# Optimization experiments

Measured on AMD Instinct MI355X. Metric: run time of the kernel, lower is better.

Reference implementation:

```python
import jax, jax.numpy as jnp
import numpy as np
import math

B, D, NH, NS, NT = 16, 256, 512, 8, 32
NV = NS * NT          # 256 prediction variables
L, H, A = 4, 8, 64    # attention layers, heads, head dim
HA = H * A            # 512
M = 512               # mlp_dim
R = 128               # resolution
EPS = 1e-5


def setup_inputs() -> dict:
    key = jax.random.key(0)
    ks = jax.random.split(key, 32)
    s = 0.02
    inp = {
        'hist_encoded': jax.random.normal(ks[0], (B, NH, D), jnp.float32),
        'hist_true_u': jax.random.uniform(ks[1], (B, NH), jnp.float32),
        'pred_encoded': jax.random.normal(ks[2], (B, NV, D), jnp.float32),
        'pred_true_u': jax.random.uniform(ks[3], (B, NV), jnp.float32),
        # dimension shifting layer
        'ds_w': jax.random.normal(ks[4], (D, HA), jnp.float32) * s,
        'ds_b': jnp.zeros((HA,), jnp.float32),
        # per-layer, per-head key/value creators: Linear(D+1 -> A)
        'key_w': jax.random.normal(ks[5], (L, H, D + 1, A), jnp.float32) * s,
        'key_b': jnp.zeros((L, H, A), jnp.float32),
        'val_w': jax.random.normal(ks[6], (L, H, D + 1, A), jnp.float32) * s,
        'val_b': jnp.zeros((L, H, A), jnp.float32),
        # layer norms
        'ln1_g': jnp.ones((L, HA), jnp.float32),
        'ln1_b': jnp.zeros((L, HA), jnp.float32),
        'ln2_g': jnp.ones((L, HA), jnp.float32),
        'ln2_b': jnp.zeros((L, HA), jnp.float32),
        # feed-forward (mlp_layers=2): HA->M, M->M, M->HA
        'ff_w1': jax.random.normal(ks[7], (L, HA, M), jnp.float32) * s,
        'ff_b1': jnp.zeros((L, M), jnp.float32),
        'ff_w2': jax.random.normal(ks[8], (L, M, M), jnp.float32) * s,
        'ff_b2': jnp.zeros((L, M), jnp.float32),
        'ff_w3': jax.random.normal(ks[9], (L, M, HA), jnp.float32) * s,
        'ff_b3': jnp.zeros((L, HA), jnp.float32),
        # dist extractor
        'de_w': jax.random.normal(ks[10], (HA, R), jnp.float32) * s,
        'de_b': jnp.zeros((R,), jnp.float32),
        'num_series': NS,
        'num_timesteps': NT,
    }
    return inp


def _ln(x, g, b):
    m = x.mean(-1, keepdims=True)
    v = ((x - m) ** 2).mean(-1, keepdims=True)
    return g * (x - m) / jnp.sqrt(v + EPS) + b


def _forward(hist_encoded, hist_true_u, pred_encoded, pred_true_u,
             ds_w, ds_b, key_w, key_b, val_w, val_b,
             ln1_g, ln1_b, ln2_g, ln2_b,
             ff_w1, ff_b1, ff_w2, ff_b2, ff_w3, ff_b3,
             de_w, de_b):
    Bm, NVm, Dm = pred_encoded.shape
    NHm = hist_encoded.shape[1]
    Lm, Hm, _, Am = key_w.shape
    W = NHm + NVm
    # identity permutation in the source loss() -> no-op
    att = pred_encoded @ ds_w + ds_b  # [B, NV, HA]
    # key/value inputs: [hist||u ; pred||u] -> [B, W, D+1]
    ki = jnp.concatenate([
        jnp.concatenate([hist_encoded, hist_true_u[:, :, None]], axis=2),
        jnp.concatenate([pred_encoded, pred_true_u[:, :, None]], axis=2)], axis=1)
    keys = jnp.einsum('bwd,lhda->lbhwa', ki, key_w) + key_b[:, None, :, None, :]
    vals = jnp.einsum('bwd,lhda->lbhwa', ki, val_w) + val_b[:, None, :, None, :]
    # flipped-triangular mask: position w is masked iff w >= NH + v
    mask = jnp.arange(W)[None, :] >= (NHm + jnp.arange(NVm)[:, None])  # [NV, W]
    scale = Am ** (-0.5)
    for l in range(Lm):
        avh = att.reshape(Bm, NVm, Hm, Am)
        prod = jnp.einsum('bvhi,bhwi->bhvw', avh, keys[l])  # [B,H,NV,W]
        prod = jnp.where(mask, -jnp.inf, prod) * scale
        w = jax.nn.softmax(prod, axis=-1)
        a = jnp.einsum('bhvw,bhwj->bvhj', w, vals[l]).reshape(Bm, NVm, Hm * Am)
        att = _ln(att + a, ln1_g[l], ln1_b[l])
        ff = jnp.maximum(att @ ff_w1[l] + ff_b1[l], 0.0)
        ff = jnp.maximum(ff @ ff_w2[l] + ff_b2[l], 0.0)
        ff = ff @ ff_w3[l] + ff_b3[l]
        att = _ln(att + ff, ln2_g[l], ln2_b[l])
    res = de_w.shape[-1]
    target = jnp.clip(jnp.floor(pred_true_u[:, 1:] * res).astype(jnp.int32), 0, res - 1)
    logits = (att @ de_w + de_b)[:, 1:, :]
    lp = math.log(res) + jax.nn.log_softmax(logits, axis=2)
    lp = jnp.take_along_axis(lp, target[:, :, None], axis=2)[:, :, 0]
    return -lp.sum(axis=1)  # [B]


def reference(hist_encoded, hist_true_u, pred_encoded, pred_true_u,
              ds_w, ds_b, key_w, key_b, val_w, val_b,
              ln1_g, ln1_b, ln2_g, ln2_b,
              ff_w1, ff_b1, ff_w2, ff_b2, ff_w3, ff_b3,
              de_w, de_b, num_series, num_timesteps):
    assert pred_encoded.shape[1] == num_series * num_timesteps
    return _forward(hist_encoded, hist_true_u, pred_encoded, pred_true_u,
                    ds_w, ds_b, key_w, key_b, val_w, val_b,
                    ln1_g, ln1_b, ln2_g, ln2_b,
                    ff_w1, ff_b1, ff_w2, ff_b2, ff_w3, ff_b3,
                    de_w, de_b)
```

## Files before the change

kernel.cpp:

```cpp
#include <hip/hip_runtime.h>

constexpr int kB = 16, kD = 256, kNH = 512, kNV = 256, kW = 768;
constexpr int kL = 4, kH = 8, kA = 64, kHA = 512, kM = 512, kR = 128;
constexpr int kKP = 288;

typedef __bf16 bf16x8 __attribute__((ext_vector_type(8)));
typedef __bf16 bf16x4 __attribute__((ext_vector_type(4)));
typedef float f32x4 __attribute__((ext_vector_type(4)));

__device__ inline void load_lds16(const __bf16* g, __bf16* l) {
  __builtin_amdgcn_global_load_lds(
      (const __attribute__((address_space(1))) void*)g,
      (__attribute__((address_space(3))) void*)l, 16, 0, 0);
}

constexpr int kP1 = kB * kW * kKP;
constexpr int kP2 = 4096 * kKP;
constexpr int kP3 = 12 * 512 * 512;
constexpr int kP4 = 200704;
constexpr int kPT = kP1 + kP2 + kP3 + kP4;

__global__ void prep_kernel(const float* __restrict__ hist,
                            const float* __restrict__ hist_u,
                            const float* __restrict__ pred,
                            const float* __restrict__ pred_u,
                            const float* __restrict__ kw,
                            const float* __restrict__ vw,
                            const float* __restrict__ w1,
                            const float* __restrict__ w2,
                            const float* __restrict__ w3,
                            const float* __restrict__ ds_w,
                            const float* __restrict__ de_w,
                            const float* __restrict__ key_b,
                            const float* __restrict__ val_b,
                            __bf16* __restrict__ ki,
                            __bf16* __restrict__ kvwt,
                            __bf16* __restrict__ ffwt,
                            __bf16* __restrict__ ds_wt,
                            __bf16* __restrict__ de_wt,
                            float* __restrict__ kvb) {
  int i = blockIdx.x * 256 + threadIdx.x;
  if (i < kP1) {
    int d = i % kKP;
    int bw = i / kKP;
    int w = bw % kW;
    int b = bw / kW;
    float v = 0.f;
    if (d < 257) {
      if (w < kNH)
        v = (d < kD) ? hist[((size_t)b * kNH + w) * kD + d] : hist_u[b * kNH + w];
      else {
        int p = w - kNH;
        v = (d < kD) ? pred[((size_t)b * kNV + p) * kD + d] : pred_u[b * kNV + p];
      }
    }
    ki[i] = (__bf16)v;
  } else if (i < kP1 + kP2) {
    int j = i - kP1;
    int d = j % kKP;
    int c = j / kKP;
    float v = 0.f;
    if (d < 257) {
      bool isv = c >= 2048;
      int cc = isv ? c - 2048 : c;
      int l = cc >> 9, rest = cc & 511;
      int h = rest >> 6, a = rest & 63;
      size_t src = (((size_t)l * kH + h) * 257 + d) * kA + a;
      v = isv ? vw[src] : kw[src];
    }
    kvwt[j] = (__bf16)v;
  } else if (i < kP1 + kP2 + kP3) {
    int j = i - kP1 - kP2;
    int k = j & 511;
    int n = (j >> 9) & 511;
    int mat = j >> 18;
    int l = mat / 3, which = mat % 3;
    const float* src = which == 0 ? w1 : which == 1 ? w2 : w3;
    ffwt[j] = (__bf16)src[((size_t)l * 512 + k) * 512 + n];
  } else if (i < kPT) {
    int j = i - kP1 - kP2 - kP3;
    if (j < 131072) {
      int n = j >> 8, k = j & 255;
      ds_wt[j] = (__bf16)ds_w[k * 512 + n];
    } else if (j < 196608) {
      int jj = j - 131072;
      int n = jj >> 9, k = jj & 511;
      de_wt[jj] = (__bf16)de_w[k * 128 + n];
    } else {
      int c = j - 196608;
      bool isv = c >= 2048;
      int cc = isv ? c - 2048 : c;
      int l = cc >> 9, rest = cc & 511;
      kvb[c] = isv ? val_b[l * 512 + rest] : key_b[l * 512 + rest];
    }
  }
}

template <int BN, int OMODE, bool RELU, bool KIMAP, bool BIASROW>
__global__ __launch_bounds__(256) void gemm_mfma_kernel(
    const __bf16* __restrict__ A, const __bf16* __restrict__ Bt,
    const float* __restrict__ bias, void* __restrict__ Cout,
    __bf16* __restrict__ Cout2, int M, int N, int K, int lda, int ldc) {
  constexpr int JN = BN / 32;
  constexpr int BROWS = BN / 4;
  __shared__ __bf16 As[128 * 32];
  __shared__ __bf16 Bs[BN * 32];
  const int t = threadIdx.x;
  const int wid = t >> 6;
  const int lane = t & 63;
  const int bm = blockIdx.y * 128;
  const int bn = blockIdx.x * BN;
  const int wm = (wid >> 1) * 64;
  const int wn = (wid & 1) * (BN / 2);
  const int sr = lane >> 2, sc = lane & 3;
  const int skey = (sr >> 1) & 3;
  const int abase = KIMAP ? ((bm >> 8) * 768 + 512 + (bm & 255)) : bm;
  const __bf16* Ag = A + (size_t)(abase + wid * 32 + sr) * lda + (sc ^ skey) * 8;
  const __bf16* Bg = Bt + (size_t)(bn + wid * BROWS + sr) * K + (sc ^ skey) * 8;
  __bf16* AsW = As + (wid * 32) * 32;
  __bf16* BsW = Bs + (wid * BROWS) * 32;

  f32x4 acc[4][JN] = {};
  const int q = lane >> 4, mr = lane & 15;
  const int rkey = (mr >> 1) & 3;
  for (int k0 = 0; k0 < K; k0 += 32) {
    if (k0) __syncthreads();
    load_lds16(Ag + k0, AsW);
    load_lds16(Ag + (size_t)16 * lda + k0, AsW + 16 * 32);
    load_lds16(Bg + k0, BsW);
    if (BN == 128) load_lds16(Bg + (size_t)16 * K + k0, BsW + 16 * 32);
    __syncthreads();
    bf16x8 af[4], bfr[JN];
#pragma unroll
    for (int i = 0; i < 4; ++i)
      af[i] = *(const bf16x8*)(As + (wm + i * 16 + mr) * 32 + (q ^ rkey) * 8);
#pragma unroll
    for (int j = 0; j < JN; ++j)
      bfr[j] = *(const bf16x8*)(Bs + (wn + j * 16 + mr) * 32 + (q ^ rkey) * 8);
#pragma unroll
    for (int i = 0; i < 4; ++i)
#pragma unroll
      for (int j = 0; j < JN; ++j)
        acc[i][j] = __builtin_amdgcn_mfma_f32_16x16x32_bf16(af[i], bfr[j],
                                                            acc[i][j], 0, 0, 0);
  }
#pragma unroll
  for (int j = 0; j < JN; ++j) {
    int col = bn + wn + j * 16 + mr;
    float bscol = BIASROW ? 0.f : bias[col];
#pragma unroll
    for (int i = 0; i < 4; ++i) {
      int row0 = bm + wm + i * 16 + q * 4;
#pragma unroll
      for (int r = 0; r < 4; ++r) {
        float v = acc[i][j][r] + (BIASROW ? bias[row0 + r] : bscol);
        if (RELU) v = fmaxf(v, 0.f);
        size_t idx = (size_t)(row0 + r) * ldc + col;
        if (OMODE == 0) {
          ((float*)Cout)[idx] = v;
        } else if (OMODE == 1) {
          ((__bf16*)Cout)[idx] = (__bf16)v;
        } else {
          ((float*)Cout)[idx] = v;
          Cout2[idx] = (__bf16)v;
        }
      }
    }
  }
}

__global__ __launch_bounds__(256) void attn_mfma_kernel(
    const __bf16* __restrict__ attbf, const __bf16* __restrict__ kvs_k,
    const __bf16* __restrict__ vT, __bf16* __restrict__ outbf, int l) {
  const int b = blockIdx.z, h = blockIdx.y, qt = blockIdx.x;
  __shared__ __bf16 Ks[64 * 72];
  __shared__ __bf16 Vt[64 * 72];
  __shared__ __bf16 Ps[64 * 72];
  const int t = threadIdx.x;
  const int w = t >> 6, lane = t & 63;
  const int quad = lane >> 4, mr = lane & 15;
  bf16x8 aq[2];
  {
    const __bf16* qp = attbf + ((size_t)(b * kNV + qt * 64 + w * 16 + mr) * kHA +
                                h * kA + quad * 8);
    aq[0] = *(const bf16x8*)qp;
    aq[1] = *(const bf16x8*)(qp + 32);
  }
  f32x4 o[4] = {};
  float m_ = -1e30f, l_ = 0.f;
  const int cmax = kNH + qt * 64;
  const int pr = t >> 2, pc = t & 3;
  const __bf16* kbase = kvs_k + ((size_t)(b * kW + pr) * 2048 + l * 512 + h * kA);
  const __bf16* vbase = vT + (size_t)(l * 512 + h * kA + pr) * 12288 + b * kW;
  bf16x8 kc0, kc1, vc0, vc1;
  kc0 = *(const bf16x8*)(kbase + pc * 8);
  kc1 = *(const bf16x8*)(kbase + pc * 8 + 32);
  vc0 = *(const bf16x8*)(vbase + pc * 16);
  vc1 = *(const bf16x8*)(vbase + pc * 16 + 8);
  for (int c0 = 0; c0 <= cmax; c0 += 64) {
    __syncthreads();
    *(bf16x8*)&Ks[pr * 72 + pc * 8] = kc0;
    *(bf16x8*)&Ks[pr * 72 + pc * 8 + 32] = kc1;
    *(bf16x8*)&Vt[pr * 72 + pc * 16] = vc0;
    *(bf16x8*)&Vt[pr * 72 + pc * 16 + 8] = vc1;
    __syncthreads();
    if (c0 + 64 <= cmax) {
      const __bf16* kp = kbase + (size_t)(c0 + 64) * 2048;
      const __bf16* vp = vbase + c0 + 64;
      kc0 = *(const bf16x8*)(kp + pc * 8);
      kc1 = *(const bf16x8*)(kp + pc * 8 + 32);
      vc0 = *(const bf16x8*)(vp + pc * 16);
      vc1 = *(const bf16x8*)(vp + pc * 16 + 8);
    }
    f32x4 s[4];
#pragma unroll
    for (int j = 0; j < 4; ++j) {
      bf16x8 ak0 = *(const bf16x8*)&Ks[(j * 16 + mr) * 72 + quad * 8];
      bf16x8 ak1 = *(const bf16x8*)&Ks[(j * 16 + mr) * 72 + quad * 8 + 32];
      f32x4 z = {};
      z = __builtin_amdgcn_mfma_f32_16x16x32_bf16(ak0, aq[0], z, 0, 0, 0);
      z = __builtin_amdgcn_mfma_f32_16x16x32_bf16(ak1, aq[1], z, 0, 0, 0);
      s[j] = z;
    }
    const int lim = cmax - c0;
    float sv[16], mx = -1e30f;
#pragma unroll
    for (int j = 0; j < 4; ++j)
#pragma unroll
      for (int r = 0; r < 4; ++r) {
        int p = j * 16 + quad * 4 + r;
        float x = (p < lim + mr) ? s[j][r] * 0.125f : -1e30f;
        sv[j * 4 + r] = x;
        mx = fmaxf(mx, x);
      }
    mx = fmaxf(mx, __shfl_xor(mx, 16));
    mx = fmaxf(mx, __shfl_xor(mx, 32));
    float mnew = fmaxf(m_, mx);
    float corr = __expf(m_ - mnew);
    float rs = 0.f;
#pragma unroll
    for (int i = 0; i < 16; ++i) {
      sv[i] = __expf(sv[i] - mnew);
      rs += sv[i];
    }
    rs += __shfl_xor(rs, 16);
    rs += __shfl_xor(rs, 32);
    l_ = l_ * corr + rs;
    m_ = mnew;
#pragma unroll
    for (int j = 0; j < 4; ++j) {
      bf16x4 pk = {(__bf16)sv[j * 4 + 0], (__bf16)sv[j * 4 + 1],
                   (__bf16)sv[j * 4 + 2], (__bf16)sv[j * 4 + 3]};
      *(bf16x4*)&Ps[(w * 16 + mr) * 72 + j * 16 + quad * 4] = pk;
    }
#pragma unroll
    for (int r = 0; r < 4; ++r) {
      float cr = __shfl(corr, quad * 4 + r);
#pragma unroll
      for (int j = 0; j < 4; ++j) o[j][r] *= cr;
    }
    bf16x8 ap0 = *(const bf16x8*)&Ps[(w * 16 + mr) * 72 + quad * 8];
    bf16x8 ap1 = *(const bf16x8*)&Ps[(w * 16 + mr) * 72 + quad * 8 + 32];
#pragma unroll
    for (int j = 0; j < 4; ++j) {
      bf16x8 b0 = *(const bf16x8*)&Vt[(j * 16 + mr) * 72 + quad * 8];
      bf16x8 b1 = *(const bf16x8*)&Vt[(j * 16 + mr) * 72 + quad * 8 + 32];
      o[j] = __builtin_amdgcn_mfma_f32_16x16x32_bf16(ap0, b0, o[j], 0, 0, 0);
      o[j] = __builtin_amdgcn_mfma_f32_16x16x32_bf16(ap1, b1, o[j], 0, 0, 0);
    }
  }
  float invl = 1.f / l_;
#pragma unroll
  for (int r = 0; r < 4; ++r) {
    float ir = __shfl(invl, quad * 4 + r);
    int row = b * kNV + qt * 64 + w * 16 + quad * 4 + r;
#pragma unroll
    for (int j = 0; j < 4; ++j)
      outbf[(size_t)row * kHA + h * kA + j * 16 + mr] = (__bf16)(o[j][r] * ir);
  }
}

__global__ __launch_bounds__(128) void add_ln_kernel(
    float* __restrict__ att, const __bf16* __restrict__ addbf,
    const float* __restrict__ g, const float* __restrict__ be,
    __bf16* __restrict__ attbf) {
  const int row = blockIdx.x;
  const int t = threadIdx.x;
  float4* ar = (float4*)(att + (size_t)row * kHA);
  bf16x4 dv = *(const bf16x4*)(addbf + (size_t)row * kHA + t * 4);
  float4 x = ar[t];
  x.x += (float)dv[0]; x.y += (float)dv[1];
  x.z += (float)dv[2]; x.w += (float)dv[3];
  float s = x.x + x.y + x.z + x.w;
  float sq = x.x * x.x + x.y * x.y + x.z * x.z + x.w * x.w;
  for (int o = 32; o; o >>= 1) {
    s += __shfl_xor(s, o);
    sq += __shfl_xor(sq, o);
  }
  __shared__ float red[4];
  if ((t & 63) == 0) { red[(t >> 6) * 2] = s; red[(t >> 6) * 2 + 1] = sq; }
  __syncthreads();
  float S = red[0] + red[2], Q = red[1] + red[3];
  float mean = S * (1.f / kHA);
  float inv = rsqrtf(Q * (1.f / kHA) - mean * mean + 1e-5f);
  float4 gv = ((const float4*)g)[t];
  float4 bv = ((const float4*)be)[t];
  float4 y;
  y.x = gv.x * (x.x - mean) * inv + bv.x;
  y.y = gv.y * (x.y - mean) * inv + bv.y;
  y.z = gv.z * (x.z - mean) * inv + bv.z;
  y.w = gv.w * (x.w - mean) * inv + bv.w;
  ar[t] = y;
  bf16x4 yb = {(__bf16)y.x, (__bf16)y.y, (__bf16)y.z, (__bf16)y.w};
  *(bf16x4*)(attbf + (size_t)row * kHA + t * 4) = yb;
}

__global__ __launch_bounds__(256) void de_loss_kernel(
    const __bf16* __restrict__ attbf, const __bf16* __restrict__ de_wt,
    const float* __restrict__ de_b, const float* __restrict__ pred_u,
    float* __restrict__ parts) {
  const int blk = blockIdx.x;
  const int t = threadIdx.x;
  const int w = t >> 6, lane = t & 63, quad = lane >> 4, mr = lane & 15;
  const int row0 = blk * 64 + w * 16;
  f32x4 acc[8] = {};
  const __bf16* Ap = attbf + (size_t)(row0 + mr) * kHA + quad * 8;
#pragma unroll 4
  for (int k0 = 0; k0 < 512; k0 += 32) {
    bf16x8 a = *(const bf16x8*)(Ap + k0);
#pragma unroll
    for (int j = 0; j < 8; ++j) {
      bf16x8 bb =
          *(const bf16x8*)(de_wt + (size_t)(j * 16 + mr) * 512 + k0 + quad * 8);
      acc[j] = __builtin_amdgcn_mfma_f32_16x16x32_bf16(a, bb, acc[j], 0, 0, 0);
    }
  }
  float dbv[8];
#pragma unroll
  for (int j = 0; j < 8; ++j) dbv[j] = de_b[j * 16 + mr];
  float lpacc = 0.f;
#pragma unroll
  for (int r = 0; r < 4; ++r) {
    int row = row0 + quad * 4 + r;
    int v = row & 255, bidx = row >> 8;
    float lg[8], mx = -1e30f;
#pragma unroll
    for (int j = 0; j < 8; ++j) {
      lg[j] = acc[j][r] + dbv[j];
      mx = fmaxf(mx, lg[j]);
    }
    mx = fmaxf(mx, __shfl_xor(mx, 1));
    mx = fmaxf(mx, __shfl_xor(mx, 2));
    mx = fmaxf(mx, __shfl_xor(mx, 4));
    mx = fmaxf(mx, __shfl_xor(mx, 8));
    float se = 0.f;
#pragma unroll
    for (int j = 0; j < 8; ++j) se += __expf(lg[j] - mx);
    se += __shfl_xor(se, 1);
    se += __shfl_xor(se, 2);
    se += __shfl_xor(se, 4);
    se += __shfl_xor(se, 8);
    float lse = mx + __logf(se);
    float u = pred_u[bidx * 256 + v];
    int tgt = (int)floorf(u * 128.f);
    tgt = max(0, min(127, tgt));
    float cand = (mr == (tgt & 15)) ? lg[tgt >> 4] : 0.f;
    cand += __shfl_xor(cand, 1);
    cand += __shfl_xor(cand, 2);
    cand += __shfl_xor(cand, 4);
    cand += __shfl_xor(cand, 8);
    float lp = (v >= 1) ? (4.8520302639196171f + cand - lse) : 0.f;
    lpacc += lp;
  }
  lpacc += __shfl_xor(lpacc, 16);
  lpacc += __shfl_xor(lpacc, 32);
  __shared__ float red[4];
  if (lane == 0) red[w] = lpacc;
  __syncthreads();
  if (t == 0) parts[blk] = red[0] + red[1] + red[2] + red[3];
}

__global__ void loss_final_kernel(const float* __restrict__ parts,
                                  float* __restrict__ out) {
  int b = threadIdx.x;
  if (b < kB)
    out[b] = -(parts[b * 4] + parts[b * 4 + 1] + parts[b * 4 + 2] +
               parts[b * 4 + 3]);
}

extern "C" void kernel_launch(void* const* d_in, const int* in_sizes, int n_in,
                              void* d_out, int out_size, void* d_ws, size_t ws_size,
                              hipStream_t stream) {
  const float* hist   = (const float*)d_in[0];
  const float* hist_u = (const float*)d_in[1];
  const float* pred   = (const float*)d_in[2];
  const float* pred_u = (const float*)d_in[3];
  const float* ds_w   = (const float*)d_in[4];
  const float* ds_b   = (const float*)d_in[5];
  const float* key_w  = (const float*)d_in[6];
  const float* key_b  = (const float*)d_in[7];
  const float* val_w  = (const float*)d_in[8];
  const float* val_b  = (const float*)d_in[9];
  const float* ln1_g  = (const float*)d_in[10];
  const float* ln1_b  = (const float*)d_in[11];
  const float* ln2_g  = (const float*)d_in[12];
  const float* ln2_b  = (const float*)d_in[13];
  const float* ff_w1  = (const float*)d_in[14];
  const float* ff_b1  = (const float*)d_in[15];
  const float* ff_w2  = (const float*)d_in[16];
  const float* ff_b2  = (const float*)d_in[17];
  const float* ff_w3  = (const float*)d_in[18];
  const float* ff_b3  = (const float*)d_in[19];
  const float* de_w   = (const float*)d_in[20];
  const float* de_b   = (const float*)d_in[21];
  float* out = (float*)d_out;

  char* ws = (char*)d_ws;
  size_t off = 0;
  auto alloc = [&](size_t bytes) { char* p = ws + off; off += bytes; return p; };
  __bf16* ki_bf  = (__bf16*)alloc((size_t)kB * kW * kKP * 2);
  __bf16* kv_wt  = (__bf16*)alloc((size_t)4096 * kKP * 2);
  __bf16* ffw_t  = (__bf16*)alloc((size_t)12 * 512 * 512 * 2);
  __bf16* ds_wt  = (__bf16*)alloc((size_t)512 * 256 * 2);
  __bf16* de_wt  = (__bf16*)alloc((size_t)128 * 512 * 2);
  float*  kvb    = (float*)alloc((size_t)4096 * 4);
  __bf16* kvs_k  = (__bf16*)alloc((size_t)kB * kW * 2048 * 2);
  __bf16* vT     = (__bf16*)alloc((size_t)2048 * 12288 * 2);
  float*  att    = (float*)alloc((size_t)kB * kNV * kHA * 4);
  __bf16* att_bf = (__bf16*)alloc((size_t)kB * kNV * kHA * 2);
  __bf16* tmp_bf = (__bf16*)alloc((size_t)kB * kNV * kHA * 2);
  __bf16* ff1_bf = (__bf16*)alloc((size_t)kB * kNV * kM * 2);
  __bf16* ff2_bf = (__bf16*)alloc((size_t)kB * kNV * kM * 2);
  float*  parts  = (float*)alloc(64 * 4);

  prep_kernel<<<(kPT + 255) / 256, 256, 0, stream>>>(
      hist, hist_u, pred, pred_u, key_w, val_w, ff_w1, ff_w2, ff_w3, ds_w, de_w,
      key_b, val_b, ki_bf, kv_wt, ffw_t, ds_wt, de_wt, kvb);

  gemm_mfma_kernel<64, 2, false, true, false>
      <<<dim3(kHA / 64, kB * kNV / 128), 256, 0, stream>>>(
          ki_bf, ds_wt, ds_b, att, att_bf, kB * kNV, kHA, kD, kKP, kHA);

  gemm_mfma_kernel<128, 1, false, false, false>
      <<<dim3(2048 / 128, kB * kW / 128), 256, 0, stream>>>(
          ki_bf, kv_wt, kvb, kvs_k, nullptr, kB * kW, 2048, kKP, kKP, 2048);
  gemm_mfma_kernel<128, 1, false, false, true>
      <<<dim3(kB * kW / 128, 2048 / 128), 256, 0, stream>>>(
          kv_wt + (size_t)2048 * kKP, ki_bf, kvb + 2048, vT, nullptr, 2048,
          kB * kW, kKP, kKP, kB * kW);

  for (int l = 0; l < kL; ++l) {
    attn_mfma_kernel<<<dim3(kNV / 64, kH, kB), 256, 0, stream>>>(
        att_bf, kvs_k, vT, tmp_bf, l);
    add_ln_kernel<<<kB * kNV, 128, 0, stream>>>(att, tmp_bf, ln1_g + l * kHA,
                                                ln1_b + l * kHA, att_bf);
    gemm_mfma_kernel<64, 1, true, false, false>
        <<<dim3(kM / 64, kB * kNV / 128), 256, 0, stream>>>(
            att_bf, ffw_t + (size_t)(l * 3) * 262144, ff_b1 + l * kM, ff1_bf,
            nullptr, kB * kNV, kM, kHA, kHA, kM);
    gemm_mfma_kernel<64, 1, true, false, false>
        <<<dim3(kM / 64, kB * kNV / 128), 256, 0, stream>>>(
            ff1_bf, ffw_t + (size_t)(l * 3 + 1) * 262144, ff_b2 + l * kM, ff2_bf,
            nullptr, kB * kNV, kM, kM, kM, kM);
    gemm_mfma_kernel<64, 1, false, false, false>
        <<<dim3(kHA / 64, kB * kNV / 128), 256, 0, stream>>>(
            ff2_bf, ffw_t + (size_t)(l * 3 + 2) * 262144, ff_b3 + l * kHA, tmp_bf,
            nullptr, kB * kNV, kHA, kM, kM, kHA);
    add_ln_kernel<<<kB * kNV, 128, 0, stream>>>(att, tmp_bf, ln2_g + l * kHA,
                                                ln2_b + l * kHA, att_bf);
  }
  de_loss_kernel<<<64, 256, 0, stream>>>(att_bf, de_wt, de_b, pred_u, parts);
  loss_final_kernel<<<1, 64, 0, stream>>>(parts, out);
}
```

Before: 492.3 us.

## Fuse layer norms into neighboring kernels via atomic row statistics

Removes the standalone add+layernorm kernels. Residual adds now happen in the attention and FF3 epilogues, which accumulate per-row sum and sum-of-squares with atomics. Normalization is applied lazily when the next consumer (attention query load, FF1 A-operand, loss kernel) reads the fp32 state, and the three initial projection GEMMs are merged into one launch. This cuts launches and bf16 round-trip traffic, at the cost of recomputing normalization in operand loads, FF1 reading fp32 A directly from global without LDS staging, and variance computed as E[x^2]-m^2.

```diff
diff --git a/kernel.cpp b/kernel.cpp
--- a/kernel.cpp
+++ b/kernel.cpp
@@ -3,6 +3,7 @@
 constexpr int kB = 16, kD = 256, kNH = 512, kNV = 256, kW = 768;
 constexpr int kL = 4, kH = 8, kA = 64, kHA = 512, kM = 512, kR = 128;
 constexpr int kKP = 288;
+constexpr int kRows = kB * kNV;
 
 typedef __bf16 bf16x8 __attribute__((ext_vector_type(8)));
 typedef __bf16 bf16x4 __attribute__((ext_vector_type(4)));
@@ -18,7 +19,8 @@
 constexpr int kP2 = 4096 * kKP;
 constexpr int kP3 = 12 * 512 * 512;
 constexpr int kP4 = 200704;
-constexpr int kPT = kP1 + kP2 + kP3 + kP4;
+constexpr int kP5 = 65536;
+constexpr int kPT = kP1 + kP2 + kP3 + kP4 + kP5;
 
 __global__ void prep_kernel(const float* __restrict__ hist,
                             const float* __restrict__ hist_u,
@@ -38,7 +40,8 @@
                             __bf16* __restrict__ ffwt,
                             __bf16* __restrict__ ds_wt,
                             __bf16* __restrict__ de_wt,
-                            float* __restrict__ kvb) {
+                            float* __restrict__ kvb,
+                            float* __restrict__ stats) {
   int i = blockIdx.x * 256 + threadIdx.x;
   if (i < kP1) {
     int d = i % kKP;
@@ -77,7 +80,7 @@
     int l = mat / 3, which = mat % 3;
     const float* src = which == 0 ? w1 : which == 1 ? w2 : w3;
     ffwt[j] = (__bf16)src[((size_t)l * 512 + k) * 512 + n];
-  } else if (i < kPT) {
+  } else if (i < kP1 + kP2 + kP3 + kP4) {
     int j = i - kP1 - kP2 - kP3;
     if (j < 131072) {
       int n = j >> 8, k = j & 255;
@@ -93,23 +96,24 @@
       int l = cc >> 9, rest = cc & 511;
       kvb[c] = isv ? val_b[l * 512 + rest] : key_b[l * 512 + rest];
     }
+  } else if (i < kPT) {
+    stats[i - kP1 - kP2 - kP3 - kP4] = 0.f;
   }
 }
 
 template <int BN, int OMODE, bool RELU, bool KIMAP, bool BIASROW>
-__global__ __launch_bounds__(256) void gemm_mfma_kernel(
-    const __bf16* __restrict__ A, const __bf16* __restrict__ Bt,
-    const float* __restrict__ bias, void* __restrict__ Cout,
-    __bf16* __restrict__ Cout2, int M, int N, int K, int lda, int ldc) {
+__device__ __forceinline__ void gemm_core(
+    int bxv, int byv, const __bf16* __restrict__ A,
+    const __bf16* __restrict__ Bt, const float* __restrict__ bias,
+    void* __restrict__ Cout, int K, int lda, int ldc,
+    __bf16* As, __bf16* Bs) {
   constexpr int JN = BN / 32;
   constexpr int BROWS = BN / 4;
-  __shared__ __bf16 As[128 * 32];
-  __shared__ __bf16 Bs[BN * 32];
   const int t = threadIdx.x;
   const int wid = t >> 6;
   const int lane = t & 63;
-  const int bm = blockIdx.y * 128;
-  const int bn = blockIdx.x * BN;
+  const int bm = byv * 128;
+  const int bn = bxv * BN;
   const int wm = (wid >> 1) * 64;
   const int wn = (wid & 1) * (BN / 2);
   const int sr = lane >> 2, sc = lane & 3;
@@ -156,22 +160,45 @@
         float v = acc[i][j][r] + (BIASROW ? bias[row0 + r] : bscol);
         if (RELU) v = fmaxf(v, 0.f);
         size_t idx = (size_t)(row0 + r) * ldc + col;
-        if (OMODE == 0) {
+        if (OMODE == 0)
           ((float*)Cout)[idx] = v;
-        } else if (OMODE == 1) {
+        else
           ((__bf16*)Cout)[idx] = (__bf16)v;
-        } else {
-          ((float*)Cout)[idx] = v;
-          Cout2[idx] = (__bf16)v;
-        }
       }
     }
   }
 }
 
-__global__ __launch_bounds__(256) void attn_mfma_kernel(
-    const __bf16* __restrict__ attbf, const __bf16* __restrict__ kvs_k,
-    const __bf16* __restrict__ vT, __bf16* __restrict__ outbf, int l) {
+__global__ __launch_bounds__(256) void gemm3_kernel(
+    const __bf16* __restrict__ ki, const __bf16* __restrict__ ds_wt,
+    const float* __restrict__ ds_b, float* __restrict__ S,
+    const __bf16* __restrict__ kv_wt, const float* __restrict__ kvb,
+    __bf16* __restrict__ kvs_k, __bf16* __restrict__ vT) {
+  __shared__ __bf16 smem[8192];
+  __bf16* As = smem;
+  __bf16* Bs = smem + 4096;
+  int bid = blockIdx.x;
+  if (bid < 256) {
+    gemm_core<64, 0, false, true, false>(bid & 7, bid >> 3, ki, ds_wt, ds_b, S,
+                                         256, kKP, 512, As, Bs);
+  } else if (bid < 1792) {
+    int b2 = bid - 256;
+    gemm_core<128, 1, false, false, false>(b2 & 15, b2 >> 4, ki, kv_wt, kvb,
+                                           kvs_k, kKP, kKP, 2048, As, Bs);
+  } else {
+    int b3 = bid - 1792;
+    gemm_core<128, 1, false, false, true>(b3 % 96, b3 / 96,
+                                          kv_wt + (size_t)2048 * kKP, ki,
+                                          kvb + 2048, vT, kKP, kKP, 12288, As,
+                                          Bs);
+  }
+}
+
+__global__ __launch_bounds__(256) void attn_kernel(
+    float* __restrict__ S, const __bf16* __restrict__ kvs_k,
+    const __bf16* __restrict__ vT, const float* __restrict__ statsPrev,
+    float* __restrict__ statsA, const float* __restrict__ g2,
+    const float* __restrict__ b2, int l) {
   const int b = blockIdx.z, h = blockIdx.y, qt = blockIdx.x;
   __shared__ __bf16 Ks[64 * 72];
   __shared__ __bf16 Vt[64 * 72];
@@ -181,10 +208,30 @@
   const int quad = lane >> 4, mr = lane & 15;
   bf16x8 aq[2];
   {
-    const __bf16* qp = attbf + ((size_t)(b * kNV + qt * 64 + w * 16 + mr) * kHA +
-                                h * kA + quad * 8);
-    aq[0] = *(const bf16x8*)qp;
-    aq[1] = *(const bf16x8*)(qp + 32);
+    int row = b * kNV + qt * 64 + w * 16 + mr;
+    const float* sp = S + (size_t)row * kHA + h * kA + quad * 8;
+    float4 x0 = *(const float4*)sp;
+    float4 x1 = *(const float4*)(sp + 4);
+    float4 x2 = *(const float4*)(sp + 32);
+    float4 x3 = *(const float4*)(sp + 36);
+    float xs[16] = {x0.x, x0.y, x0.z, x0.w, x1.x, x1.y, x1.z, x1.w,
+                    x2.x, x2.y, x2.z, x2.w, x3.x, x3.y, x3.z, x3.w};
+    if (l > 0) {
+      float s0 = statsPrev[2 * row], s1 = statsPrev[2 * row + 1];
+      float m = s0 * (1.f / kHA);
+      float inv = rsqrtf(s1 * (1.f / kHA) - m * m + 1e-5f);
+      int cbase = h * kA + quad * 8;
+#pragma unroll
+      for (int e = 0; e < 8; ++e) {
+        xs[e] = (xs[e] - m) * inv * g2[cbase + e] + b2[cbase + e];
+        xs[8 + e] = (xs[8 + e] - m) * inv * g2[cbase + 32 + e] + b2[cbase + 32 + e];
+      }
+    }
+#pragma unroll
+    for (int e = 0; e < 8; ++e) {
+      aq[0][e] = (__bf16)xs[e];
+      aq[1][e] = (__bf16)xs[8 + e];
+    }
   }
   f32x4 o[4] = {};
   float m_ = -1e30f, l_ = 0.f;
@@ -274,60 +321,248 @@
   for (int r = 0; r < 4; ++r) {
     float ir = __shfl(invl, quad * 4 + r);
     int row = b * kNV + qt * 64 + w * 16 + quad * 4 + r;
-#pragma unroll
-    for (int j = 0; j < 4; ++j)
-      outbf[(size_t)row * kHA + h * kA + j * 16 + mr] = (__bf16)(o[j][r] * ir);
-  }
-}
-
-__global__ __launch_bounds__(128) void add_ln_kernel(
-    float* __restrict__ att, const __bf16* __restrict__ addbf,
+    float m = 0.f, inv = 0.f;
+    if (l > 0) {
+      float s0 = statsPrev[2 * row], s1 = statsPrev[2 * row + 1];
+      m = s0 * (1.f / kHA);
+      inv = rsqrtf(s1 * (1.f / kHA) - m * m + 1e-5f);
+    }
+    float ps = 0.f, pq = 0.f;
+#pragma unroll
+    for (int j = 0; j < 4; ++j) {
+      int col = h * kA + j * 16 + mr;
+      size_t idx = (size_t)row * kHA + col;
+      float sval = S[idx];
+      float base = (l > 0) ? ((sval - m) * inv * g2[col] + b2[col]) : sval;
+      float v = base + o[j][r] * ir;
+      S[idx] = v;
+      ps += v;
+      pq += v * v;
+    }
+    ps += __shfl_xor(ps, 1); pq += __shfl_xor(pq, 1);
+    ps += __shfl_xor(ps, 2); pq += __shfl_xor(pq, 2);
+    ps += __shfl_xor(ps, 4); pq += __shfl_xor(pq, 4);
+    ps += __shfl_xor(ps, 8); pq += __shfl_xor(pq, 8);
+    if (mr == 0) {
+      atomicAdd(&statsA[2 * row], ps);
+      atomicAdd(&statsA[2 * row + 1], pq);
+    }
+  }
+}
+
+__global__ __launch_bounds__(256) void ff1_ln_gemm_kernel(
+    const float* __restrict__ S, const float* __restrict__ stats,
     const float* __restrict__ g, const float* __restrict__ be,
-    __bf16* __restrict__ attbf) {
-  const int row = blockIdx.x;
+    const __bf16* __restrict__ Bt, const float* __restrict__ bias,
+    __bf16* __restrict__ Cout) {
+  __shared__ __bf16 Bs[64 * 32];
+  __shared__ float gb[1024];
   const int t = threadIdx.x;
-  float4* ar = (float4*)(att + (size_t)row * kHA);
-  bf16x4 dv = *(const bf16x4*)(addbf + (size_t)row * kHA + t * 4);
-  float4 x = ar[t];
-  x.x += (float)dv[0]; x.y += (float)dv[1];
-  x.z += (float)dv[2]; x.w += (float)dv[3];
-  float s = x.x + x.y + x.z + x.w;
-  float sq = x.x * x.x + x.y * x.y + x.z * x.z + x.w * x.w;
-  for (int o = 32; o; o >>= 1) {
-    s += __shfl_xor(s, o);
-    sq += __shfl_xor(sq, o);
-  }
-  __shared__ float red[4];
-  if ((t & 63) == 0) { red[(t >> 6) * 2] = s; red[(t >> 6) * 2 + 1] = sq; }
+  for (int i = t; i < 512; i += 256) {
+    gb[i] = g[i];
+    gb[512 + i] = be[i];
+  }
+  const int wid = t >> 6, lane = t & 63;
+  const int quad = lane >> 4, mr = lane & 15;
+  const int bm = blockIdx.y * 128, bn = blockIdx.x * 64;
+  const int wm = (wid >> 1) * 64, wn = (wid & 1) * 32;
+  const int sr = lane >> 2, sc = lane & 3;
+  const int skey = (sr >> 1) & 3;
+  const __bf16* Bg = Bt + (size_t)(bn + wid * 16 + sr) * 512 + (sc ^ skey) * 8;
+  __bf16* BsW = Bs + (wid * 16) * 32;
+  float mean_[4], inv_[4];
+#pragma unroll
+  for (int i = 0; i < 4; ++i) {
+    int row = bm + wm + i * 16 + mr;
+    float s0 = stats[2 * row], s1 = stats[2 * row + 1];
+    float m = s0 * (1.f / kHA);
+    mean_[i] = m;
+    inv_[i] = rsqrtf(s1 * (1.f / kHA) - m * m + 1e-5f);
+  }
+  const int rkey = (mr >> 1) & 3;
+  f32x4 acc[4][2] = {};
   __syncthreads();
-  float S = red[0] + red[2], Q = red[1] + red[3];
-  float mean = S * (1.f / kHA);
-  float inv = rsqrtf(Q * (1.f / kHA) - mean * mean + 1e-5f);
-  float4 gv = ((const float4*)g)[t];
-  float4 bv = ((const float4*)be)[t];
-  float4 y;
-  y.x = gv.x * (x.x - mean) * inv + bv.x;
-  y.y = gv.y * (x.y - mean) * inv + bv.y;
-  y.z = gv.z * (x.z - mean) * inv + bv.z;
-  y.w = gv.w * (x.w - mean) * inv + bv.w;
-  ar[t] = y;
-  bf16x4 yb = {(__bf16)y.x, (__bf16)y.y, (__bf16)y.z, (__bf16)y.w};
-  *(bf16x4*)(attbf + (size_t)row * kHA + t * 4) = yb;
+  for (int k0 = 0; k0 < 512; k0 += 32) {
+    if (k0) __syncthreads();
+    load_lds16(Bg + k0, BsW);
+    __syncthreads();
+    const int kq = k0 + quad * 8;
+    float4 gv0 = *(const float4*)&gb[kq];
+    float4 gv1 = *(const float4*)&gb[kq + 4];
+    float4 bv0 = *(const float4*)&gb[512 + kq];
+    float4 bv1 = *(const float4*)&gb[512 + kq + 4];
+    bf16x8 af[4];
+#pragma unroll
+    for (int i = 0; i < 4; ++i) {
+      int row = bm + wm + i * 16 + mr;
+      const float* sp = S + (size_t)row * 512 + kq;
+      float4 a0 = *(const float4*)sp;
+      float4 a1 = *(const float4*)(sp + 4);
+      float m = mean_[i], rr = inv_[i];
+      bf16x8 v;
+      v[0] = (__bf16)((a0.x - m) * rr * gv0.x + bv0.x);
+      v[1] = (__bf16)((a0.y - m) * rr * gv0.y + bv0.y);
+      v[2] = (__bf16)((a0.z - m) * rr * gv0.z + bv0.z);
+      v[3] = (__bf16)((a0.w - m) * rr * gv0.w + bv0.w);
+      v[4] = (__bf16)((a1.x - m) * rr * gv1.x + bv1.x);
+      v[5] = (__bf16)((a1.y - m) * rr * gv1.y + bv1.y);
+      v[6] = (__bf16)((a1.z - m) * rr * gv1.z + bv1.z);
+      v[7] = (__bf16)((a1.w - m) * rr * gv1.w + bv1.w);
+      af[i] = v;
+    }
+    bf16x8 bfr[2];
+#pragma unroll
+    for (int j = 0; j < 2; ++j)
+      bfr[j] = *(const bf16x8*)(Bs + (wn + j * 16 + mr) * 32 + (quad ^ rkey) * 8);
+#pragma unroll
+    for (int i = 0; i < 4; ++i)
+#pragma unroll
+      for (int j = 0; j < 2; ++j)
+        acc[i][j] = __builtin_amdgcn_mfma_f32_16x16x32_bf16(af[i], bfr[j],
+                                                            acc[i][j], 0, 0, 0);
+  }
+#pragma unroll
+  for (int j = 0; j < 2; ++j) {
+    int col = bn + wn + j * 16 + mr;
+    float bs = bias[col];
+#pragma unroll
+    for (int i = 0; i < 4; ++i) {
+      int row0 = bm + wm + i * 16 + quad * 4;
+#pragma unroll
+      for (int r = 0; r < 4; ++r) {
+        float v = fmaxf(acc[i][j][r] + bs, 0.f);
+        Cout[(size_t)(row0 + r) * 512 + col] = (__bf16)v;
+      }
+    }
+  }
+}
+
+__global__ __launch_bounds__(256) void gemm_ff2_kernel(
+    const __bf16* __restrict__ A, const __bf16* __restrict__ Bt,
+    const float* __restrict__ bias, __bf16* __restrict__ Cout) {
+  __shared__ __bf16 smem[6144];
+  gemm_core<64, 1, true, false, false>(blockIdx.x, blockIdx.y, A, Bt, bias,
+                                       Cout, 512, 512, 512, smem, smem + 4096);
+}
+
+__global__ __launch_bounds__(256) void ff3_res_gemm_kernel(
+    const __bf16* __restrict__ A, const __bf16* __restrict__ Bt,
+    const float* __restrict__ bias, float* __restrict__ S,
+    const float* __restrict__ statsA, float* __restrict__ statsB,
+    const float* __restrict__ g1, const float* __restrict__ b1) {
+  __shared__ __bf16 As[128 * 32];
+  __shared__ __bf16 Bs[64 * 32];
+  __shared__ float gb1[128];
+  const int t = threadIdx.x;
+  const int wid = t >> 6, lane = t & 63;
+  const int quad = lane >> 4, mr = lane & 15;
+  const int bm = blockIdx.y * 128, bn = blockIdx.x * 64;
+  const int wm = (wid >> 1) * 64, wn = (wid & 1) * 32;
+  if (t < 64) {
+    gb1[t] = g1[bn + t];
+    gb1[64 + t] = b1[bn + t];
+  }
+  const int sr = lane >> 2, sc = lane & 3;
+  const int skey = (sr >> 1) & 3;
+  const __bf16* Ag = A + (size_t)(bm + wid * 32 + sr) * 512 + (sc ^ skey) * 8;
+  const __bf16* Bg = Bt + (size_t)(bn + wid * 16 + sr) * 512 + (sc ^ skey) * 8;
+  __bf16* AsW = As + (wid * 32) * 32;
+  __bf16* BsW = Bs + (wid * 16) * 32;
+  f32x4 acc[4][2] = {};
+  const int rkey = (mr >> 1) & 3;
+  for (int k0 = 0; k0 < 512; k0 += 32) {
+    if (k0) __syncthreads();
+    load_lds16(Ag + k0, AsW);
+    load_lds16(Ag + (size_t)16 * 512 + k0, AsW + 16 * 32);
+    load_lds16(Bg + k0, BsW);
+    __syncthreads();
+    bf16x8 af[4], bfr[2];
+#pragma unroll
+    for (int i = 0; i < 4; ++i)
+      af[i] = *(const bf16x8*)(As + (wm + i * 16 + mr) * 32 + (quad ^ rkey) * 8);
+#pragma unroll
+    for (int j = 0; j < 2; ++j)
+      bfr[j] = *(const bf16x8*)(Bs + (wn + j * 16 + mr) * 32 + (quad ^ rkey) * 8);
+#pragma unroll
+    for (int i = 0; i < 4; ++i)
+#pragma unroll
+      for (int j = 0; j < 2; ++j)
+        acc[i][j] = __builtin_amdgcn_mfma_f32_16x16x32_bf16(af[i], bfr[j],
+                                                            acc[i][j], 0, 0, 0);
+  }
+#pragma unroll
+  for (int i = 0; i < 4; ++i) {
+    int row0 = bm + wm + i * 16 + quad * 4;
+#pragma unroll
+    for (int r = 0; r < 4; ++r) {
+      int row = row0 + r;
+      float s0 = statsA[2 * row], s1 = statsA[2 * row + 1];
+      float m = s0 * (1.f / kHA);
+      float inv = rsqrtf(s1 * (1.f / kHA) - m * m + 1e-5f);
+      float ps = 0.f, pq = 0.f;
+#pragma unroll
+      for (int j = 0; j < 2; ++j) {
+        int lc = wn + j * 16 + mr;
+        int col = bn + lc;
+        size_t idx = (size_t)row * 512 + col;
+        float sval = S[idx];
+        float resid = (sval - m) * inv * gb1[lc] + gb1[64 + lc];
+        float v = resid + acc[i][j][r] + bias[col];
+        S[idx] = v;
+        ps += v;
+        pq += v * v;
+      }
+      ps += __shfl_xor(ps, 1); pq += __shfl_xor(pq, 1);
+      ps += __shfl_xor(ps, 2); pq += __shfl_xor(pq, 2);
+      ps += __shfl_xor(ps, 4); pq += __shfl_xor(pq, 4);
+      ps += __shfl_xor(ps, 8); pq += __shfl_xor(pq, 8);
+      if (mr == 0) {
+        atomicAdd(&statsB[2 * row], ps);
+        atomicAdd(&statsB[2 * row + 1], pq);
+      }
+    }
+  }
 }
 
 __global__ __launch_bounds__(256) void de_loss_kernel(
-    const __bf16* __restrict__ attbf, const __bf16* __restrict__ de_wt,
-    const float* __restrict__ de_b, const float* __restrict__ pred_u,
-    float* __restrict__ parts) {
+    const float* __restrict__ S, const float* __restrict__ stats,
+    const float* __restrict__ g2, const float* __restrict__ b2,
+    const __bf16* __restrict__ de_wt, const float* __restrict__ de_b,
+    const float* __restrict__ pred_u, float* __restrict__ parts) {
+  __shared__ float gb[1024];
   const int blk = blockIdx.x;
   const int t = threadIdx.x;
+  for (int i = t; i < 512; i += 256) {
+    gb[i] = g2[i];
+    gb[512 + i] = b2[i];
+  }
+  __syncthreads();
   const int w = t >> 6, lane = t & 63, quad = lane >> 4, mr = lane & 15;
   const int row0 = blk * 64 + w * 16;
+  const int arow = row0 + mr;
+  float s0 = stats[2 * arow], s1 = stats[2 * arow + 1];
+  float m = s0 * (1.f / kHA);
+  float inv = rsqrtf(s1 * (1.f / kHA) - m * m + 1e-5f);
   f32x4 acc[8] = {};
-  const __bf16* Ap = attbf + (size_t)(row0 + mr) * kHA + quad * 8;
-#pragma unroll 4
+#pragma unroll 2
   for (int k0 = 0; k0 < 512; k0 += 32) {
-    bf16x8 a = *(const bf16x8*)(Ap + k0);
+    const int kq = k0 + quad * 8;
+    const float* sp = S + (size_t)arow * 512 + kq;
+    float4 a0 = *(const float4*)sp;
+    float4 a1 = *(const float4*)(sp + 4);
+    float4 gv0 = *(const float4*)&gb[kq];
+    float4 gv1 = *(const float4*)&gb[kq + 4];
+    float4 bv0 = *(const float4*)&gb[512 + kq];
+    float4 bv1 = *(const float4*)&gb[512 + kq + 4];
+    bf16x8 a;
+    a[0] = (__bf16)((a0.x - m) * inv * gv0.x + bv0.x);
+    a[1] = (__bf16)((a0.y - m) * inv * gv0.y + bv0.y);
+    a[2] = (__bf16)((a0.z - m) * inv * gv0.z + bv0.z);
+    a[3] = (__bf16)((a0.w - m) * inv * gv0.w + bv0.w);
+    a[4] = (__bf16)((a1.x - m) * inv * gv1.x + bv1.x);
+    a[5] = (__bf16)((a1.y - m) * inv * gv1.y + bv1.y);
+    a[6] = (__bf16)((a1.z - m) * inv * gv1.z + bv1.z);
+    a[7] = (__bf16)((a1.w - m) * inv * gv1.w + bv1.w);
 #pragma unroll
     for (int j = 0; j < 8; ++j) {
       bf16x8 bb =
@@ -426,49 +661,38 @@
   float*  kvb    = (float*)alloc((size_t)4096 * 4);
   __bf16* kvs_k  = (__bf16*)alloc((size_t)kB * kW * 2048 * 2);
   __bf16* vT     = (__bf16*)alloc((size_t)2048 * 12288 * 2);
-  float*  att    = (float*)alloc((size_t)kB * kNV * kHA * 4);
-  __bf16* att_bf = (__bf16*)alloc((size_t)kB * kNV * kHA * 2);
-  __bf16* tmp_bf = (__bf16*)alloc((size_t)kB * kNV * kHA * 2);
-  __bf16* ff1_bf = (__bf16*)alloc((size_t)kB * kNV * kM * 2);
-  __bf16* ff2_bf = (__bf16*)alloc((size_t)kB * kNV * kM * 2);
+  float*  S      = (float*)alloc((size_t)kRows * kHA * 4);
+  float*  stats  = (float*)alloc((size_t)kP5 * 4);
+  __bf16* ff1_bf = (__bf16*)alloc((size_t)kRows * kM * 2);
+  __bf16* ff2_bf = (__bf16*)alloc((size_t)kRows * kM * 2);
   float*  parts  = (float*)alloc(64 * 4);
 
   prep_kernel<<<(kPT + 255) / 256, 256, 0, stream>>>(
       hist, hist_u, pred, pred_u, key_w, val_w, ff_w1, ff_w2, ff_w3, ds_w, de_w,
-      key_b, val_b, ki_bf, kv_wt, ffw_t, ds_wt, de_wt, kvb);
-
-  gemm_mfma_kernel<64, 2, false, true, false>
-      <<<dim3(kHA / 64, kB * kNV / 128), 256, 0, stream>>>(
-          ki_bf, ds_wt, ds_b, att, att_bf, kB * kNV, kHA, kD, kKP, kHA);
-
-  gemm_mfma_kernel<128, 1, false, false, false>
-      <<<dim3(2048 / 128, kB * kW / 128), 256, 0, stream>>>(
-          ki_bf, kv_wt, kvb, kvs_k, nullptr, kB * kW, 2048, kKP, kKP, 2048);
-  gemm_mfma_kernel<128, 1, false, false, true>
-      <<<dim3(kB * kW / 128, 2048 / 128), 256, 0, stream>>>(
-          kv_wt + (size_t)2048 * kKP, ki_bf, kvb + 2048, vT, nullptr, 2048,
-          kB * kW, kKP, kKP, kB * kW);
+      key_b, val_b, ki_bf, kv_wt, ffw_t, ds_wt, de_wt, kvb, stats);
+
+  gemm3_kernel<<<3328, 256, 0, stream>>>(ki_bf, ds_wt, ds_b, S, kv_wt, kvb,
+                                         kvs_k, vT);
 
   for (int l = 0; l < kL; ++l) {
-    attn_mfma_kernel<<<dim3(kNV / 64, kH, kB), 256, 0, stream>>>(
-        att_bf, kvs_k, vT, tmp_bf, l);
-    add_ln_kernel<<<kB * kNV, 128, 0, stream>>>(att, tmp_bf, ln1_g + l * kHA,
-                                                ln1_b + l * kHA, att_bf);
-    gemm_mfma_kernel<64, 1, true, false, false>
-        <<<dim3(kM / 64, kB * kNV / 128), 256, 0, stream>>>(
-            att_bf, ffw_t + (size_t)(l * 3) * 262144, ff_b1 + l * kM, ff1_bf,
-            nullptr, kB * kNV, kM, kHA, kHA, kM);
-    gemm_mfma_kernel<64, 1, true, false, false>
-        <<<dim3(kM / 64, kB * kNV / 128), 256, 0, stream>>>(
-            ff1_bf, ffw_t + (size_t)(l * 3 + 1) * 262144, ff_b2 + l * kM, ff2_bf,
-            nullptr, kB * kNV, kM, kM, kM, kM);
-    gemm_mfma_kernel<64, 1, false, false, false>
-        <<<dim3(kHA / 64, kB * kNV / 128), 256, 0, stream>>>(
-            ff2_bf, ffw_t + (size_t)(l * 3 + 2) * 262144, ff_b3 + l * kHA, tmp_bf,
-            nullptr, kB * kNV, kHA, kM, kM, kHA);
-    add_ln_kernel<<<kB * kNV, 128, 0, stream>>>(att, tmp_bf, ln2_g + l * kHA,
-                                                ln2_b + l * kHA, att_bf);
-  }
-  de_loss_kernel<<<64, 256, 0, stream>>>(att_bf, de_wt, de_b, pred_u, parts);
+    float* statsA = stats + l * 8192;
+    float* statsB = stats + 32768 + l * 8192;
+    const float* statsPrev = stats + 32768 + (l - 1) * 8192;
+    attn_kernel<<<dim3(kNV / 64, kH, kB), 256, 0, stream>>>(
+        S, kvs_k, vT, (l > 0) ? statsPrev : stats, statsA,
+        ln2_g + (l > 0 ? (l - 1) : 0) * kHA, ln2_b + (l > 0 ? (l - 1) : 0) * kHA,
+        l);
+    ff1_ln_gemm_kernel<<<dim3(kM / 64, kRows / 128), 256, 0, stream>>>(
+        S, statsA, ln1_g + l * kHA, ln1_b + l * kHA,
+        ffw_t + (size_t)(l * 3) * 262144, ff_b1 + l * kM, ff1_bf);
+    gemm_ff2_kernel<<<dim3(kM / 64, kRows / 128), 256, 0, stream>>>(
+        ff1_bf, ffw_t + (size_t)(l * 3 + 1) * 262144, ff_b2 + l * kM, ff2_bf);
+    ff3_res_gemm_kernel<<<dim3(kHA / 64, kRows / 128), 256, 0, stream>>>(
+        ff2_bf, ffw_t + (size_t)(l * 3 + 2) * 262144, ff_b3 + l * kHA, S,
+        statsA, statsB, ln1_g + l * kHA, ln1_b + l * kHA);
+  }
+  de_loss_kernel<<<64, 256, 0, stream>>>(S, stats + 32768 + 3 * 8192,
+                                         ln2_g + 3 * kHA, ln2_b + 3 * kHA, de_wt,
+                                         de_b, pred_u, parts);
   loss_final_kernel<<<1, 64, 0, stream>>>(parts, out);
 }
```

After: 577.4 us. 17.3% more time.
